# Optimization experiments

Hardware: AMD Instinct MI355X
Metric: run time of the kernel (lower is better)

The kernel has to match this reference:

```python
import math
import jax, jax.numpy as jnp
import numpy as np

B, L, D, H = 4, 2048, 1024, 16
HS = D // H  # 64


def setup_inputs() -> dict:
    key = jax.random.key(0)
    ks = jax.random.split(key, 6)
    x = jax.random.normal(ks[0], (B, L, D), dtype=jnp.float32)
    W_attn = jax.random.normal(ks[1], (D, 3 * D), dtype=jnp.float32) * 0.02
    b_attn = jnp.zeros((3 * D,), dtype=jnp.float32)
    W_proj = jax.random.normal(ks[2], (D, D), dtype=jnp.float32) * 0.02
    b_proj = jnp.zeros((D,), dtype=jnp.float32)
    Er = jax.random.normal(ks[3], (L, HS), dtype=jnp.float32)  # block_size == L
    return {"x": x, "W_attn": W_attn, "b_attn": b_attn,
            "W_proj": W_proj, "b_proj": b_proj, "Er": Er}


def _skew(QEr):
    # QEr: [B, H, L, L] -> pad one column on the left, reshape, drop first row.
    b, h, r, c = QEr.shape
    padded = jnp.pad(QEr, ((0, 0), (0, 0), (0, 0), (1, 0)))  # [B,H,L,L+1]
    return padded.reshape(b, h, c + 1, r)[:, :, 1:, :]        # [B,H,L,L]


def reference(x, W_attn, b_attn, W_proj, b_proj, Er):
    b, l, d = x.shape
    qkv = x @ W_attn + b_attn                     # [B,L,3D]
    q, k, v = jnp.split(qkv, 3, axis=2)
    q = q.reshape(b, l, H, HS).transpose(0, 2, 1, 3)  # [B,H,L,hs]
    k = k.reshape(b, l, H, HS).transpose(0, 2, 1, 3)
    v = v.reshape(b, l, H, HS).transpose(0, 2, 1, 3)
    # start = block_size - L = 0 here; Er_t: [hs, L]
    Er_t = Er[Er.shape[0] - l:, :].T
    QEr = jnp.einsum('bhld,dm->bhlm', q, Er_t)    # [B,H,L,L]
    Srel = _skew(QEr)
    scale = 1.0 / math.sqrt(HS)
    att = (jnp.einsum('bhqd,bhkd->bhqk', q, k) + Srel) * scale
    causal = jnp.tril(jnp.ones((l, l), dtype=bool))
    att = jnp.where(causal[None, None, :, :], att, -jnp.inf)
    att = jax.nn.softmax(att, axis=-1)
    y = jnp.einsum('bhqk,bhkd->bhqd', att, v)     # [B,H,L,hs]
    y = y.transpose(0, 2, 1, 3).reshape(b, l, d)
    return y @ W_proj + b_proj
```

## Files before the change

### kernel.cpp

```cpp
#include <hip/hip_runtime.h>
#include <hip/hip_bf16.h>
#include <math.h>

#define B_  4
#define L_  2048
#define D_  1024
#define H_  16
#define HS_ 64
#define SCALE 0.125f

typedef unsigned short ushort_t;
typedef __attribute__((ext_vector_type(8))) short short8;
typedef __attribute__((ext_vector_type(4))) float f32x4;

static __device__ __forceinline__ ushort_t f2bf(float f) {
    union { float f; unsigned int u; } cv; cv.f = f;
    unsigned int u = cv.u;
    unsigned int r = (u + 0x7FFFu + ((u >> 16) & 1u)) >> 16;
    return (ushort_t)r;
}
static __device__ __forceinline__ float bf2f(ushort_t h) {
    union { float f; unsigned int u; } cv; cv.u = ((unsigned int)h) << 16;
    return cv.f;
}

static __device__ __forceinline__ void gload_lds16(const ushort_t* g, ushort_t* l) {
    __builtin_amdgcn_global_load_lds(
        (const __attribute__((address_space(1))) unsigned int*)g,
        (__attribute__((address_space(3))) unsigned int*)l, 16, 0, 0);
}

__global__ __launch_bounds__(256)
void conv_to_bf16(const float* __restrict__ x, ushort_t* __restrict__ xb)
{
    const size_t i = (size_t)blockIdx.x * 256 + threadIdx.x;
    const float4* src = (const float4*)x + i * 2;
    float4 a = src[0], b = src[1];
    ushort_t o[8] = {f2bf(a.x), f2bf(a.y), f2bf(a.z), f2bf(a.w),
                     f2bf(b.x), f2bf(b.y), f2bf(b.z), f2bf(b.w)};
    *(uint4*)(xb + i * 8) = *(uint4*)o;
}

__global__ __launch_bounds__(256)
void transpose_to_bf16(const float* __restrict__ W, ushort_t* __restrict__ Wt,
                       int K, int N)
{
    __shared__ ushort_t tile[64][65];
    const int tid = threadIdx.x;
    const int n0 = blockIdx.x * 64, k0 = blockIdx.y * 64;
#pragma unroll
    for (int s = 0; s < 16; ++s) {
        const int idx = s * 256 + tid;
        const int kl = idx >> 6, nl = idx & 63;
        tile[nl][kl] = f2bf(W[(size_t)(k0 + kl) * N + n0 + nl]);
    }
    __syncthreads();
#pragma unroll
    for (int s = 0; s < 8; ++s) {
        const int idx = s * 256 + tid;
        const int nl = idx >> 5, kc = idx & 31;
        const unsigned int vlo = tile[nl][kc * 2];
        const unsigned int vhi = tile[nl][kc * 2 + 1];
        *(unsigned int*)(Wt + (size_t)(n0 + nl) * K + k0 + kc * 2) =
            vlo | (vhi << 16);
    }
}

__global__ __launch_bounds__(256)
void qkv_mfma(const ushort_t* __restrict__ A, const ushort_t* __restrict__ Bt,
              const float* __restrict__ bias, ushort_t* __restrict__ qkv)
{
    __shared__ __align__(16) ushort_t As[128 * 64];
    __shared__ __align__(16) ushort_t Bs[128 * 64];

    const int tid = threadIdx.x;
    const int w = tid >> 6, lane = tid & 63, quad = lane >> 4, lcol = lane & 15;
    const int wr = w >> 1, wc = w & 1;
    const int m0 = blockIdx.y * 128, n0 = blockIdx.x * 128;
    const int K = D_;

    const int srow = tid >> 3;
    const int cg = (tid & 7) ^ (srow & 7);
    const ushort_t* gA = A + (size_t)(m0 + srow) * K + cg * 8;
    const ushort_t* gB = Bt + (size_t)(n0 + srow) * K + cg * 8;
    ushort_t* lA = As + tid * 8;
    ushort_t* lB = Bs + tid * 8;

    const int cs0 = ((quad) ^ (lcol & 7)) * 8;
    const int cs1 = ((4 + quad) ^ (lcol & 7)) * 8;

    f32x4 acc[4][4];
#pragma unroll
    for (int i = 0; i < 4; ++i)
#pragma unroll
        for (int j = 0; j < 4; ++j) acc[i][j] = (f32x4){0, 0, 0, 0};

    for (int k0 = 0; k0 < K; k0 += 64) {
        __syncthreads();
#pragma unroll
        for (int s = 0; s < 4; ++s) {
            gload_lds16(gA + k0 + (size_t)s * 32 * K, lA + s * 2048);
            gload_lds16(gB + k0 + (size_t)s * 32 * K, lB + s * 2048);
        }
        __syncthreads();
#pragma unroll
        for (int kk = 0; kk < 2; ++kk) {
            const int cs = kk ? cs1 : cs0;
            short8 af[4], bf[4];
#pragma unroll
            for (int i = 0; i < 4; ++i)
                af[i] = *(const short8*)&As[(wr * 64 + i * 16 + lcol) * 64 + cs];
#pragma unroll
            for (int j = 0; j < 4; ++j)
                bf[j] = *(const short8*)&Bs[(wc * 64 + j * 16 + lcol) * 64 + cs];
#pragma unroll
            for (int i = 0; i < 4; ++i)
#pragma unroll
                for (int j = 0; j < 4; ++j)
                    acc[i][j] = __builtin_amdgcn_mfma_f32_16x16x32_bf16(
                        af[i], bf[j], acc[i][j], 0, 0, 0);
        }
    }

    const size_t per = (size_t)B_ * H_ * L_ * HS_;
#pragma unroll
    for (int j = 0; j < 4; ++j) {
        const int col = n0 + wc * 64 + j * 16 + lcol;
        const float bv = bias[col];
        const int sel = col >> 10;
        const int within = col & 1023;
        const int hh = within >> 6, hs = within & 63;
        ushort_t* base = qkv + (size_t)sel * per;
#pragma unroll
        for (int i = 0; i < 4; ++i) {
#pragma unroll
            for (int reg = 0; reg < 4; ++reg) {
                const int row = m0 + wr * 64 + i * 16 + quad * 4 + reg;
                const int bb = row >> 11, ll = row & 2047;
                base[(((size_t)(bb * H_ + hh)) * L_ + ll) * HS_ + hs] =
                    f2bf(acc[i][j][reg] + bv);
            }
        }
    }
}

__global__ __launch_bounds__(256)
void proj_mfma(const ushort_t* __restrict__ A, const ushort_t* __restrict__ Bt,
               const float* __restrict__ bias, float* __restrict__ C)
{
    __shared__ __align__(16) ushort_t As[128 * 64];
    __shared__ __align__(16) ushort_t Bs[128 * 64];

    const int tid = threadIdx.x;
    const int w = tid >> 6, lane = tid & 63, quad = lane >> 4, lcol = lane & 15;
    const int wr = w >> 1, wc = w & 1;
    const int m0 = blockIdx.y * 128, n0 = blockIdx.x * 128;
    const int K = D_;
    const int N = D_;

    const int srow = tid >> 3;
    const int cg = (tid & 7) ^ (srow & 7);
    const ushort_t* gA = A + (size_t)(m0 + srow) * K + cg * 8;
    const ushort_t* gB = Bt + (size_t)(n0 + srow) * K + cg * 8;
    ushort_t* lA = As + tid * 8;
    ushort_t* lB = Bs + tid * 8;

    const int cs0 = ((quad) ^ (lcol & 7)) * 8;
    const int cs1 = ((4 + quad) ^ (lcol & 7)) * 8;

    f32x4 acc[4][4];
#pragma unroll
    for (int i = 0; i < 4; ++i)
#pragma unroll
        for (int j = 0; j < 4; ++j) acc[i][j] = (f32x4){0, 0, 0, 0};

    for (int k0 = 0; k0 < K; k0 += 64) {
        __syncthreads();
#pragma unroll
        for (int s = 0; s < 4; ++s) {
            gload_lds16(gA + k0 + (size_t)s * 32 * K, lA + s * 2048);
            gload_lds16(gB + k0 + (size_t)s * 32 * K, lB + s * 2048);
        }
        __syncthreads();
#pragma unroll
        for (int kk = 0; kk < 2; ++kk) {
            const int cs = kk ? cs1 : cs0;
            short8 af[4], bf[4];
#pragma unroll
            for (int i = 0; i < 4; ++i)
                af[i] = *(const short8*)&As[(wr * 64 + i * 16 + lcol) * 64 + cs];
#pragma unroll
            for (int j = 0; j < 4; ++j)
                bf[j] = *(const short8*)&Bs[(wc * 64 + j * 16 + lcol) * 64 + cs];
#pragma unroll
            for (int i = 0; i < 4; ++i)
#pragma unroll
                for (int j = 0; j < 4; ++j)
                    acc[i][j] = __builtin_amdgcn_mfma_f32_16x16x32_bf16(
                        af[i], bf[j], acc[i][j], 0, 0, 0);
        }
    }

#pragma unroll
    for (int j = 0; j < 4; ++j) {
        const int col = n0 + wc * 64 + j * 16 + lcol;
        const float bv = bias[col];
#pragma unroll
        for (int i = 0; i < 4; ++i) {
#pragma unroll
            for (int reg = 0; reg < 4; ++reg) {
                const int row = m0 + wr * 64 + i * 16 + quad * 4 + reg;
                C[(size_t)row * N + col] = acc[i][j][reg] + bv;
            }
        }
    }
}

#define QT 64
#define KT 64

__global__ __launch_bounds__(256)
void attn_mfma(const ushort_t* __restrict__ q, const ushort_t* __restrict__ k,
               const ushort_t* __restrict__ v, const float* __restrict__ Er,
               ushort_t* __restrict__ y)
{
    __shared__ __align__(16) ushort_t Qs[64][72];
    __shared__ __align__(16) ushort_t Ks[64][72];
    __shared__ __align__(16) ushort_t Vt[64][72];
    __shared__ __align__(16) ushort_t EsPs[64][72];
    __shared__ __align__(16) ushort_t EBuf[64][132];

    const int tid  = threadIdx.x;
    const int w    = tid >> 6;
    const int lane = tid & 63;
    const int quad = lane >> 4;
    const int lcol = lane & 15;
    const int bh   = blockIdx.y;
    const int qt   = (int)gridDim.x - 1 - (int)blockIdx.x;
    const int qi0  = qt * QT;
    const int bb   = bh >> 4;
    const int hh   = bh & 15;
    const int cband = L_ - QT - qi0;

    const ushort_t* qp = q + (size_t)bh * L_ * HS_;
    const ushort_t* kp = k + (size_t)bh * L_ * HS_;
    const ushort_t* vp = v + (size_t)bh * L_ * HS_;

    const int srow = tid >> 2;
    const int scol = (tid & 3) * 16;

    {
        const uint4* src = (const uint4*)(qp + (size_t)(qi0 + srow) * HS_ + scol);
        *(uint4*)&Qs[srow][scol]     = src[0];
        *(uint4*)&Qs[srow][scol + 8] = src[1];
    }
    {
        const int m = cband + srow;
        const float4* src = (const float4*)(Er + (size_t)m * HS_ + scol);
        float4 f0 = src[0], f1 = src[1], f2 = src[2], f3 = src[3];
        ushort_t o[16];
        o[0]=f2bf(f0.x); o[1]=f2bf(f0.y); o[2]=f2bf(f0.z); o[3]=f2bf(f0.w);
        o[4]=f2bf(f1.x); o[5]=f2bf(f1.y); o[6]=f2bf(f1.z); o[7]=f2bf(f1.w);
        o[8]=f2bf(f2.x); o[9]=f2bf(f2.y); o[10]=f2bf(f2.z); o[11]=f2bf(f2.w);
        o[12]=f2bf(f3.x); o[13]=f2bf(f3.y); o[14]=f2bf(f3.z); o[15]=f2bf(f3.w);
        *(uint4*)&EsPs[srow][scol]     = *(uint4*)&o[0];
        *(uint4*)&EsPs[srow][scol + 8] = *(uint4*)&o[8];
    }
    __syncthreads();

    const short8 aq0 = *(const short8*)&Qs[w * 16 + lcol][quad * 8];
    const short8 aq1 = *(const short8*)&Qs[w * 16 + lcol][32 + quad * 8];

    {
        f32x4 e0 = {0,0,0,0}, e1 = {0,0,0,0}, e2 = {0,0,0,0}, e3 = {0,0,0,0};
        e0 = __builtin_amdgcn_mfma_f32_16x16x32_bf16(aq0, *(const short8*)&EsPs[ 0 + lcol][quad*8],      e0, 0,0,0);
        e1 = __builtin_amdgcn_mfma_f32_16x16x32_bf16(aq0, *(const short8*)&EsPs[16 + lcol][quad*8],      e1, 0,0,0);
        e2 = __builtin_amdgcn_mfma_f32_16x16x32_bf16(aq0, *(const short8*)&EsPs[32 + lcol][quad*8],      e2, 0,0,0);
        e3 = __builtin_amdgcn_mfma_f32_16x16x32_bf16(aq0, *(const short8*)&EsPs[48 + lcol][quad*8],      e3, 0,0,0);
        e0 = __builtin_amdgcn_mfma_f32_16x16x32_bf16(aq1, *(const short8*)&EsPs[ 0 + lcol][32 + quad*8], e0, 0,0,0);
        e1 = __builtin_amdgcn_mfma_f32_16x16x32_bf16(aq1, *(const short8*)&EsPs[16 + lcol][32 + quad*8], e1, 0,0,0);
        e2 = __builtin_amdgcn_mfma_f32_16x16x32_bf16(aq1, *(const short8*)&EsPs[32 + lcol][32 + quad*8], e2, 0,0,0);
        e3 = __builtin_amdgcn_mfma_f32_16x16x32_bf16(aq1, *(const short8*)&EsPs[48 + lcol][32 + quad*8], e3, 0,0,0);
        const int rw = w * 16 + quad * 4;
#pragma unroll
        for (int reg = 0; reg < 4; ++reg) {
            EBuf[rw + reg][ 0 + lcol] = f2bf(e0[reg]);
            EBuf[rw + reg][16 + lcol] = f2bf(e1[reg]);
            EBuf[rw + reg][32 + lcol] = f2bf(e2[reg]);
            EBuf[rw + reg][48 + lcol] = f2bf(e3[reg]);
        }
    }

    f32x4 O[4];
#pragma unroll
    for (int nt = 0; nt < 4; ++nt) O[nt] = (f32x4){0, 0, 0, 0};
    float m_r[4] = {-INFINITY, -INFINITY, -INFINITY, -INFINITY};
    float l_r[4] = {0, 0, 0, 0};

    for (int kt = 0; kt <= qt; ++kt) {
        const int kj0 = kt * KT;
        __syncthreads();

        {
            const uint4* src = (const uint4*)(kp + (size_t)(kj0 + srow) * HS_ + scol);
            *(uint4*)&Ks[srow][scol]     = src[0];
            *(uint4*)&Ks[srow][scol + 8] = src[1];
        }
        {
            const ushort_t* src = vp + (size_t)(kj0 + srow) * HS_ + scol;
            uint4 a = *(const uint4*)src, b = *(const uint4*)(src + 8);
            ushort_t tmp[16];
            *(uint4*)&tmp[0] = a; *(uint4*)&tmp[8] = b;
#pragma unroll
            for (int u = 0; u < 16; ++u) Vt[scol + u][srow] = tmp[u];
        }
        {
            int m = cband + (kt + 1) * 64 + srow;
            m = (m > L_ - 1) ? (L_ - 1) : m;
            const float4* src = (const float4*)(Er + (size_t)m * HS_ + scol);
            float4 f0 = src[0], f1 = src[1], f2 = src[2], f3 = src[3];
            ushort_t o[16];
            o[0]=f2bf(f0.x); o[1]=f2bf(f0.y); o[2]=f2bf(f0.z); o[3]=f2bf(f0.w);
            o[4]=f2bf(f1.x); o[5]=f2bf(f1.y); o[6]=f2bf(f1.z); o[7]=f2bf(f1.w);
            o[8]=f2bf(f2.x); o[9]=f2bf(f2.y); o[10]=f2bf(f2.z); o[11]=f2bf(f2.w);
            o[12]=f2bf(f3.x); o[13]=f2bf(f3.y); o[14]=f2bf(f3.z); o[15]=f2bf(f3.w);
            *(uint4*)&EsPs[srow][scol]     = *(uint4*)&o[0];
            *(uint4*)&EsPs[srow][scol + 8] = *(uint4*)&o[8];
        }
        __syncthreads();

        f32x4 s0 = {0,0,0,0}, s1 = {0,0,0,0}, s2 = {0,0,0,0}, s3 = {0,0,0,0};
        f32x4 e0 = {0,0,0,0}, e1 = {0,0,0,0}, e2 = {0,0,0,0}, e3 = {0,0,0,0};
        s0 = __builtin_amdgcn_mfma_f32_16x16x32_bf16(aq0, *(const short8*)&Ks[ 0 + lcol][quad*8],        s0, 0,0,0);
        s1 = __builtin_amdgcn_mfma_f32_16x16x32_bf16(aq0, *(const short8*)&Ks[16 + lcol][quad*8],        s1, 0,0,0);
        s2 = __builtin_amdgcn_mfma_f32_16x16x32_bf16(aq0, *(const short8*)&Ks[32 + lcol][quad*8],        s2, 0,0,0);
        s3 = __builtin_amdgcn_mfma_f32_16x16x32_bf16(aq0, *(const short8*)&Ks[48 + lcol][quad*8],        s3, 0,0,0);
        s0 = __builtin_amdgcn_mfma_f32_16x16x32_bf16(aq1, *(const short8*)&Ks[ 0 + lcol][32 + quad*8],   s0, 0,0,0);
        s1 = __builtin_amdgcn_mfma_f32_16x16x32_bf16(aq1, *(const short8*)&Ks[16 + lcol][32 + quad*8],   s1, 0,0,0);
        s2 = __builtin_amdgcn_mfma_f32_16x16x32_bf16(aq1, *(const short8*)&Ks[32 + lcol][32 + quad*8],   s2, 0,0,0);
        s3 = __builtin_amdgcn_mfma_f32_16x16x32_bf16(aq1, *(const short8*)&Ks[48 + lcol][32 + quad*8],   s3, 0,0,0);
        e0 = __builtin_amdgcn_mfma_f32_16x16x32_bf16(aq0, *(const short8*)&EsPs[ 0 + lcol][quad*8],      e0, 0,0,0);
        e1 = __builtin_amdgcn_mfma_f32_16x16x32_bf16(aq0, *(const short8*)&EsPs[16 + lcol][quad*8],      e1, 0,0,0);
        e2 = __builtin_amdgcn_mfma_f32_16x16x32_bf16(aq0, *(const short8*)&EsPs[32 + lcol][quad*8],      e2, 0,0,0);
        e3 = __builtin_amdgcn_mfma_f32_16x16x32_bf16(aq0, *(const short8*)&EsPs[48 + lcol][quad*8],      e3, 0,0,0);
        e0 = __builtin_amdgcn_mfma_f32_16x16x32_bf16(aq1, *(const short8*)&EsPs[ 0 + lcol][32 + quad*8], e0, 0,0,0);
        e1 = __builtin_amdgcn_mfma_f32_16x16x32_bf16(aq1, *(const short8*)&EsPs[16 + lcol][32 + quad*8], e1, 0,0,0);
        e2 = __builtin_amdgcn_mfma_f32_16x16x32_bf16(aq1, *(const short8*)&EsPs[32 + lcol][32 + quad*8], e2, 0,0,0);
        e3 = __builtin_amdgcn_mfma_f32_16x16x32_bf16(aq1, *(const short8*)&EsPs[48 + lcol][32 + quad*8], e3, 0,0,0);

        {
            const int par = ((kt + 1) & 1) * 64;
            const int rw = w * 16 + quad * 4;
#pragma unroll
            for (int reg = 0; reg < 4; ++reg) {
                EBuf[rw + reg][par +  0 + lcol] = f2bf(e0[reg]);
                EBuf[rw + reg][par + 16 + lcol] = f2bf(e1[reg]);
                EBuf[rw + reg][par + 32 + lcol] = f2bf(e2[reg]);
                EBuf[rw + reg][par + 48 + lcol] = f2bf(e3[reg]);
            }
        }

        float p_[4][4];
        float al[4];
        const float sq[4][4] = {
            {s0[0], s0[1], s0[2], s0[3]},
            {s1[0], s1[1], s1[2], s1[3]},
            {s2[0], s2[1], s2[2], s2[3]},
            {s3[0], s3[1], s3[2], s3[3]}};
#pragma unroll
        for (int reg = 0; reg < 4; ++reg) {
            const int r = w * 16 + quad * 4 + reg;
            float scr[4];
#pragma unroll
            for (int nt = 0; nt < 4; ++nt) {
                const int jl = nt * 16 + lcol;
                const int c = (63 - r + jl + kj0) & 127;
                float sv = (sq[nt][reg] + bf2f(EBuf[r][c])) * SCALE;
                if (kt == qt && jl > r) sv = -INFINITY;
                scr[nt] = sv;
            }
            float mx = fmaxf(fmaxf(scr[0], scr[1]), fmaxf(scr[2], scr[3]));
            mx = fmaxf(mx, __shfl_xor(mx, 1));
            mx = fmaxf(mx, __shfl_xor(mx, 2));
            mx = fmaxf(mx, __shfl_xor(mx, 4));
            mx = fmaxf(mx, __shfl_xor(mx, 8));
            const float nm = fmaxf(m_r[reg], mx);
            const float a_ = __expf(m_r[reg] - nm);
            m_r[reg] = nm;
            float ps = 0.f;
#pragma unroll
            for (int nt = 0; nt < 4; ++nt) {
                const float p = __expf(scr[nt] - nm);
                p_[nt][reg] = p;
                ps += p;
            }
            ps += __shfl_xor(ps, 1);
            ps += __shfl_xor(ps, 2);
            ps += __shfl_xor(ps, 4);
            ps += __shfl_xor(ps, 8);
            l_r[reg] = l_r[reg] * a_ + ps;
            al[reg] = a_;
        }
#pragma unroll
        for (int nt = 0; nt < 4; ++nt)
#pragma unroll
            for (int reg = 0; reg < 4; ++reg) O[nt][reg] *= al[reg];

        __syncthreads();

        {
            const int rw = w * 16 + quad * 4;
#pragma unroll
            for (int reg = 0; reg < 4; ++reg) {
                EsPs[rw + reg][ 0 + lcol] = f2bf(p_[0][reg]);
                EsPs[rw + reg][16 + lcol] = f2bf(p_[1][reg]);
                EsPs[rw + reg][32 + lcol] = f2bf(p_[2][reg]);
                EsPs[rw + reg][48 + lcol] = f2bf(p_[3][reg]);
            }
        }
        const short8 ap0 = *(const short8*)&EsPs[w * 16 + lcol][quad * 8];
        const short8 ap1 = *(const short8*)&EsPs[w * 16 + lcol][32 + quad * 8];
        O[0] = __builtin_amdgcn_mfma_f32_16x16x32_bf16(ap0, *(const short8*)&Vt[ 0 + lcol][quad*8],      O[0], 0,0,0);
        O[1] = __builtin_amdgcn_mfma_f32_16x16x32_bf16(ap0, *(const short8*)&Vt[16 + lcol][quad*8],      O[1], 0,0,0);
        O[2] = __builtin_amdgcn_mfma_f32_16x16x32_bf16(ap0, *(const short8*)&Vt[32 + lcol][quad*8],      O[2], 0,0,0);
        O[3] = __builtin_amdgcn_mfma_f32_16x16x32_bf16(ap0, *(const short8*)&Vt[48 + lcol][quad*8],      O[3], 0,0,0);
        O[0] = __builtin_amdgcn_mfma_f32_16x16x32_bf16(ap1, *(const short8*)&Vt[ 0 + lcol][32 + quad*8], O[0], 0,0,0);
        O[1] = __builtin_amdgcn_mfma_f32_16x16x32_bf16(ap1, *(const short8*)&Vt[16 + lcol][32 + quad*8], O[1], 0,0,0);
        O[2] = __builtin_amdgcn_mfma_f32_16x16x32_bf16(ap1, *(const short8*)&Vt[32 + lcol][32 + quad*8], O[2], 0,0,0);
        O[3] = __builtin_amdgcn_mfma_f32_16x16x32_bf16(ap1, *(const short8*)&Vt[48 + lcol][32 + quad*8], O[3], 0,0,0);
    }

    float inv[4];
#pragma unroll
    for (int reg = 0; reg < 4; ++reg) inv[reg] = 1.f / l_r[reg];
#pragma unroll
    for (int nt = 0; nt < 4; ++nt) {
#pragma unroll
        for (int reg = 0; reg < 4; ++reg) {
            const int r = w * 16 + quad * 4 + reg;
            y[(((size_t)bb * L_ + qi0 + r) * H_ + hh) * HS_ + nt * 16 + lcol] =
                f2bf(O[nt][reg] * inv[reg]);
        }
    }
}

extern "C" void kernel_launch(void* const* d_in, const int* in_sizes, int n_in,
                              void* d_out, int out_size, void* d_ws, size_t ws_size,
                              hipStream_t stream)
{
    const float* x      = (const float*)d_in[0];
    const float* W_attn = (const float*)d_in[1];
    const float* b_attn = (const float*)d_in[2];
    const float* W_proj = (const float*)d_in[3];
    const float* b_proj = (const float*)d_in[4];
    const float* Er     = (const float*)d_in[5];
    float* out = (float*)d_out;

    const size_t per = (size_t)B_ * H_ * L_ * HS_;
    ushort_t* qb  = (ushort_t*)d_ws;
    ushort_t* kb  = qb + per;
    ushort_t* vb  = kb + per;
    ushort_t* yb  = vb + per;
    ushort_t* xb  = yb + per;
    ushort_t* wat = xb + per;
    ushort_t* wpt = wat + (size_t)3 * D_ * D_;

    dim3 blk(256);

    conv_to_bf16<<<dim3((B_ * L_ * D_) / 2048), blk, 0, stream>>>(x, xb);
    transpose_to_bf16<<<dim3(3 * D_ / 64, D_ / 64), blk, 0, stream>>>(W_attn, wat, D_, 3 * D_);
    transpose_to_bf16<<<dim3(D_ / 64, D_ / 64), blk, 0, stream>>>(W_proj, wpt, D_, D_);

    qkv_mfma<<<dim3(3 * D_ / 128, B_ * L_ / 128), blk, 0, stream>>>(xb, wat, b_attn, qb);

    attn_mfma<<<dim3(L_ / QT, B_ * H_), blk, 0, stream>>>(qb, kb, vb, Er, yb);

    proj_mfma<<<dim3(D_ / 128, B_ * L_ / 128), blk, 0, stream>>>(yb, wpt, b_proj, out);
}
```

Measured before the change: 582.8 us.

## Restructure attention: register-ring skew, max-free softmax, transposed V, async LDS loads

The QKV epilogue now writes V already transposed, and Er is converted to bf16 once up front. K, V^T, Q and Er tiles are loaded straight into XOR-swizzled LDS with global_load_lds, replacing the per-thread transposes and float-to-bf16 conversions inside the loop. The relative-position skew is kept in a register ring of QEr tiles read through lane shuffles instead of a bf16 LDS buffer. The softmax also drops the running max and rescaling, saving one barrier and the max reductions per iteration, at the risk of exp overflow if scores grow large. The loop is unrolled by two and launch bounds request higher occupancy.

```diff
diff --git a/kernel.cpp b/kernel.cpp
--- a/kernel.cpp
+++ b/kernel.cpp
@@ -18,10 +18,6 @@
     unsigned int u = cv.u;
     unsigned int r = (u + 0x7FFFu + ((u >> 16) & 1u)) >> 16;
     return (ushort_t)r;
-}
-static __device__ __forceinline__ float bf2f(ushort_t h) {
-    union { float f; unsigned int u; } cv; cv.u = ((unsigned int)h) << 16;
-    return cv.f;
 }
 
 static __device__ __forceinline__ void gload_lds16(const ushort_t* g, ushort_t* l) {
@@ -130,15 +126,29 @@
         const int sel = col >> 10;
         const int within = col & 1023;
         const int hh = within >> 6, hs = within & 63;
-        ushort_t* base = qkv + (size_t)sel * per;
-#pragma unroll
-        for (int i = 0; i < 4; ++i) {
-#pragma unroll
-            for (int reg = 0; reg < 4; ++reg) {
-                const int row = m0 + wr * 64 + i * 16 + quad * 4 + reg;
-                const int bb = row >> 11, ll = row & 2047;
-                base[(((size_t)(bb * H_ + hh)) * L_ + ll) * HS_ + hs] =
-                    f2bf(acc[i][j][reg] + bv);
+        if (sel < 2) {
+            ushort_t* base = qkv + (size_t)sel * per;
+#pragma unroll
+            for (int i = 0; i < 4; ++i) {
+#pragma unroll
+                for (int reg = 0; reg < 4; ++reg) {
+                    const int row = m0 + wr * 64 + i * 16 + quad * 4 + reg;
+                    const int bb = row >> 11, ll = row & 2047;
+                    base[(((size_t)(bb * H_ + hh)) * L_ + ll) * HS_ + hs] =
+                        f2bf(acc[i][j][reg] + bv);
+                }
+            }
+        } else {
+            ushort_t* base = qkv + 2 * per;
+#pragma unroll
+            for (int i = 0; i < 4; ++i) {
+#pragma unroll
+                for (int reg = 0; reg < 4; ++reg) {
+                    const int row = m0 + wr * 64 + i * 16 + quad * 4 + reg;
+                    const int bb = row >> 11, ll = row & 2047;
+                    base[(((size_t)(bb * H_ + hh)) * HS_ + hs) * L_ + ll] =
+                        f2bf(acc[i][j][reg] + bv);
+                }
             }
         }
     }
@@ -216,19 +226,98 @@
     }
 }
 
-#define QT 64
-#define KT 64
-
-__global__ __launch_bounds__(256)
+#define MFMA16(a, b, c) __builtin_amdgcn_mfma_f32_16x16x32_bf16(a, b, c, 0, 0, 0)
+
+#define RING_STORE(C1) do {                                                       \
+    if (w == 0)      { Ring[((C1)+5)&7]=e0; Ring[((C1)+6)&7]=e1;                  \
+                       Ring[((C1)+7)&7]=e2; Ring[((C1)+8)&7]=e3; }                \
+    else if (w == 1) { Ring[((C1)+6)&7]=e0; Ring[((C1)+7)&7]=e1;                  \
+                       Ring[((C1)+8)&7]=e2; Ring[((C1)+9)&7]=e3; }                \
+    else if (w == 2) { Ring[((C1)+7)&7]=e0; Ring[((C1)+8)&7]=e1;                  \
+                       Ring[((C1)+9)&7]=e2; Ring[((C1)+10)&7]=e3; }               \
+    else             { Ring[((C1)+8)&7]=e0; Ring[((C1)+9)&7]=e1;                  \
+                       Ring[((C1)+10)&7]=e2; Ring[((C1)+11)&7]=e3; }              \
+} while (0)
+
+#define ATTN_ITER(KTv, C0, C1) {                                                  \
+    const int kj0 = (KTv) * 64;                                                   \
+    const bool diag = ((KTv) == qt);                                              \
+    __syncthreads();                                                              \
+    gload_lds16(kp + (size_t)(kj0 + srow) * 64 + cg8, Ks + tid * 8);              \
+    gload_lds16(kp + (size_t)(kj0 + srow + 32) * 64 + cg8, Ks + tid * 8 + 2048);  \
+    gload_lds16(vtp + (size_t)srow * L_ + kj0 + cg8, Vts + tid * 8);              \
+    gload_lds16(vtp + (size_t)(srow + 32) * L_ + kj0 + cg8, Vts + tid * 8 + 2048);\
+    { int m1 = cband + ((KTv) + 1) * 64 + srow; if (m1 > L_ - 1) m1 = L_ - 1;     \
+      int m2 = cband + ((KTv) + 1) * 64 + srow + 32; if (m2 > L_ - 1) m2 = L_ - 1;\
+      gload_lds16(er + (size_t)m1 * 64 + cg8, Es + tid * 8);                      \
+      gload_lds16(er + (size_t)m2 * 64 + cg8, Es + tid * 8 + 2048); }             \
+    __syncthreads();                                                              \
+    f32x4 S0 = {0,0,0,0}, S1 = {0,0,0,0}, S2 = {0,0,0,0}, S3 = {0,0,0,0};         \
+    f32x4 e0 = {0,0,0,0}, e1 = {0,0,0,0}, e2 = {0,0,0,0}, e3 = {0,0,0,0};         \
+    S0 = MFMA16(aq0, *(const short8*)&Ks[( 0 + lcol) * 64 + fr0], S0);            \
+    S1 = MFMA16(aq0, *(const short8*)&Ks[(16 + lcol) * 64 + fr0], S1);            \
+    S2 = MFMA16(aq0, *(const short8*)&Ks[(32 + lcol) * 64 + fr0], S2);            \
+    S3 = MFMA16(aq0, *(const short8*)&Ks[(48 + lcol) * 64 + fr0], S3);            \
+    S0 = MFMA16(aq1, *(const short8*)&Ks[( 0 + lcol) * 64 + fr1], S0);            \
+    S1 = MFMA16(aq1, *(const short8*)&Ks[(16 + lcol) * 64 + fr1], S1);            \
+    S2 = MFMA16(aq1, *(const short8*)&Ks[(32 + lcol) * 64 + fr1], S2);            \
+    S3 = MFMA16(aq1, *(const short8*)&Ks[(48 + lcol) * 64 + fr1], S3);            \
+    e0 = MFMA16(aq0, *(const short8*)&Es[( 0 + lcol) * 64 + fr0], e0);            \
+    e1 = MFMA16(aq0, *(const short8*)&Es[(16 + lcol) * 64 + fr0], e1);            \
+    e2 = MFMA16(aq0, *(const short8*)&Es[(32 + lcol) * 64 + fr0], e2);            \
+    e3 = MFMA16(aq0, *(const short8*)&Es[(48 + lcol) * 64 + fr0], e3);            \
+    e0 = MFMA16(aq1, *(const short8*)&Es[( 0 + lcol) * 64 + fr1], e0);            \
+    e1 = MFMA16(aq1, *(const short8*)&Es[(16 + lcol) * 64 + fr1], e1);            \
+    e2 = MFMA16(aq1, *(const short8*)&Es[(32 + lcol) * 64 + fr1], e2);            \
+    e3 = MFMA16(aq1, *(const short8*)&Es[(48 + lcol) * 64 + fr1], e3);            \
+    RING_STORE(C1);                                                               \
+    f32x4 S[4] = {S0, S1, S2, S3};                                                \
+    _Pragma("unroll")                                                             \
+    for (int reg = 0; reg < 4; ++reg) {                                           \
+        const int qr = quad * 4 + reg;                                            \
+        const int srcl = quad * 16 + ((15 - qr + lcol) & 15);                     \
+        const bool carry = (lcol > qr);                                           \
+        float psum = 0.f;                                                         \
+        _Pragma("unroll")                                                         \
+        for (int nt = 0; nt < 4; ++nt) {                                          \
+            const float v0 = __shfl(Ring[((C0) + nt) & 7][reg], srcl, 64);        \
+            const float v1 = __shfl(Ring[((C0) + nt + 1) & 7][reg], srcl, 64);    \
+            const float ev = carry ? v1 : v0;                                     \
+            const float sv = (S[nt][reg] + ev) * SCALE;                           \
+            float p = __expf(sv);                                                 \
+            if (diag && (nt * 16 + lcol > w * 16 + qr)) p = 0.f;                  \
+            psum += p;                                                            \
+            Ps[(w * 16 + qr) * 64 +                                               \
+               (((nt * 2 + (lcol >> 3)) ^ (qr & 7)) * 8) + (lcol & 7)] = f2bf(p); \
+        }                                                                         \
+        psum += __shfl_xor(psum, 1);                                              \
+        psum += __shfl_xor(psum, 2);                                              \
+        psum += __shfl_xor(psum, 4);                                              \
+        psum += __shfl_xor(psum, 8);                                              \
+        l_r[reg] += psum;                                                         \
+    }                                                                             \
+    const short8 ap0 = *(const short8*)&Ps[(w * 16 + lcol) * 64 + fr0];           \
+    const short8 ap1 = *(const short8*)&Ps[(w * 16 + lcol) * 64 + fr1];           \
+    O[0] = MFMA16(ap0, *(const short8*)&Vts[( 0 + lcol) * 64 + fr0], O[0]);       \
+    O[1] = MFMA16(ap0, *(const short8*)&Vts[(16 + lcol) * 64 + fr0], O[1]);       \
+    O[2] = MFMA16(ap0, *(const short8*)&Vts[(32 + lcol) * 64 + fr0], O[2]);       \
+    O[3] = MFMA16(ap0, *(const short8*)&Vts[(48 + lcol) * 64 + fr0], O[3]);       \
+    O[0] = MFMA16(ap1, *(const short8*)&Vts[( 0 + lcol) * 64 + fr1], O[0]);       \
+    O[1] = MFMA16(ap1, *(const short8*)&Vts[(16 + lcol) * 64 + fr1], O[1]);       \
+    O[2] = MFMA16(ap1, *(const short8*)&Vts[(32 + lcol) * 64 + fr1], O[2]);       \
+    O[3] = MFMA16(ap1, *(const short8*)&Vts[(48 + lcol) * 64 + fr1], O[3]);       \
+}
+
+__global__ __launch_bounds__(256, 4)
 void attn_mfma(const ushort_t* __restrict__ q, const ushort_t* __restrict__ k,
-               const ushort_t* __restrict__ v, const float* __restrict__ Er,
+               const ushort_t* __restrict__ vt, const ushort_t* __restrict__ er,
                ushort_t* __restrict__ y)
 {
-    __shared__ __align__(16) ushort_t Qs[64][72];
-    __shared__ __align__(16) ushort_t Ks[64][72];
-    __shared__ __align__(16) ushort_t Vt[64][72];
-    __shared__ __align__(16) ushort_t EsPs[64][72];
-    __shared__ __align__(16) ushort_t EBuf[64][132];
+    __shared__ __align__(16) ushort_t Qs[64 * 64];
+    __shared__ __align__(16) ushort_t Ks[64 * 64];
+    __shared__ __align__(16) ushort_t Vts[64 * 64];
+    __shared__ __align__(16) ushort_t Es[64 * 64];
+    __shared__ __align__(16) ushort_t Ps[64 * 64];
 
     const int tid  = threadIdx.x;
     const int w    = tid >> 6;
@@ -237,197 +326,51 @@
     const int lcol = lane & 15;
     const int bh   = blockIdx.y;
     const int qt   = (int)gridDim.x - 1 - (int)blockIdx.x;
-    const int qi0  = qt * QT;
+    const int qi0  = qt * 64;
     const int bb   = bh >> 4;
     const int hh   = bh & 15;
-    const int cband = L_ - QT - qi0;
-
-    const ushort_t* qp = q + (size_t)bh * L_ * HS_;
-    const ushort_t* kp = k + (size_t)bh * L_ * HS_;
-    const ushort_t* vp = v + (size_t)bh * L_ * HS_;
-
-    const int srow = tid >> 2;
-    const int scol = (tid & 3) * 16;
-
-    {
-        const uint4* src = (const uint4*)(qp + (size_t)(qi0 + srow) * HS_ + scol);
-        *(uint4*)&Qs[srow][scol]     = src[0];
-        *(uint4*)&Qs[srow][scol + 8] = src[1];
-    }
-    {
-        const int m = cband + srow;
-        const float4* src = (const float4*)(Er + (size_t)m * HS_ + scol);
-        float4 f0 = src[0], f1 = src[1], f2 = src[2], f3 = src[3];
-        ushort_t o[16];
-        o[0]=f2bf(f0.x); o[1]=f2bf(f0.y); o[2]=f2bf(f0.z); o[3]=f2bf(f0.w);
-        o[4]=f2bf(f1.x); o[5]=f2bf(f1.y); o[6]=f2bf(f1.z); o[7]=f2bf(f1.w);
-        o[8]=f2bf(f2.x); o[9]=f2bf(f2.y); o[10]=f2bf(f2.z); o[11]=f2bf(f2.w);
-        o[12]=f2bf(f3.x); o[13]=f2bf(f3.y); o[14]=f2bf(f3.z); o[15]=f2bf(f3.w);
-        *(uint4*)&EsPs[srow][scol]     = *(uint4*)&o[0];
-        *(uint4*)&EsPs[srow][scol + 8] = *(uint4*)&o[8];
-    }
+    const int cband = L_ - 64 - qi0;
+
+    const ushort_t* qp  = q + (size_t)bh * L_ * HS_;
+    const ushort_t* kp  = k + (size_t)bh * L_ * HS_;
+    const ushort_t* vtp = vt + (size_t)bh * HS_ * L_;
+
+    const int srow = tid >> 3;
+    const int cg8  = ((tid & 7) ^ (srow & 7)) * 8;
+
+    gload_lds16(qp + (size_t)(qi0 + srow) * 64 + cg8, Qs + tid * 8);
+    gload_lds16(qp + (size_t)(qi0 + srow + 32) * 64 + cg8, Qs + tid * 8 + 2048);
+    gload_lds16(er + (size_t)(cband + srow) * 64 + cg8, Es + tid * 8);
+    gload_lds16(er + (size_t)(cband + srow + 32) * 64 + cg8, Es + tid * 8 + 2048);
     __syncthreads();
 
-    const short8 aq0 = *(const short8*)&Qs[w * 16 + lcol][quad * 8];
-    const short8 aq1 = *(const short8*)&Qs[w * 16 + lcol][32 + quad * 8];
-
+    const int fr0 = ((quad) ^ (lcol & 7)) * 8;
+    const int fr1 = ((4 + quad) ^ (lcol & 7)) * 8;
+    const short8 aq0 = *(const short8*)&Qs[(w * 16 + lcol) * 64 + fr0];
+    const short8 aq1 = *(const short8*)&Qs[(w * 16 + lcol) * 64 + fr1];
+
+    f32x4 Ring[8];
     {
         f32x4 e0 = {0,0,0,0}, e1 = {0,0,0,0}, e2 = {0,0,0,0}, e3 = {0,0,0,0};
-        e0 = __builtin_amdgcn_mfma_f32_16x16x32_bf16(aq0, *(const short8*)&EsPs[ 0 + lcol][quad*8],      e0, 0,0,0);
-        e1 = __builtin_amdgcn_mfma_f32_16x16x32_bf16(aq0, *(const short8*)&EsPs[16 + lcol][quad*8],      e1, 0,0,0);
-        e2 = __builtin_amdgcn_mfma_f32_16x16x32_bf16(aq0, *(const short8*)&EsPs[32 + lcol][quad*8],      e2, 0,0,0);
-        e3 = __builtin_amdgcn_mfma_f32_16x16x32_bf16(aq0, *(const short8*)&EsPs[48 + lcol][quad*8],      e3, 0,0,0);
-        e0 = __builtin_amdgcn_mfma_f32_16x16x32_bf16(aq1, *(const short8*)&EsPs[ 0 + lcol][32 + quad*8], e0, 0,0,0);
-        e1 = __builtin_amdgcn_mfma_f32_16x16x32_bf16(aq1, *(const short8*)&EsPs[16 + lcol][32 + quad*8], e1, 0,0,0);
-        e2 = __builtin_amdgcn_mfma_f32_16x16x32_bf16(aq1, *(const short8*)&EsPs[32 + lcol][32 + quad*8], e2, 0,0,0);
-        e3 = __builtin_amdgcn_mfma_f32_16x16x32_bf16(aq1, *(const short8*)&EsPs[48 + lcol][32 + quad*8], e3, 0,0,0);
-        const int rw = w * 16 + quad * 4;
-#pragma unroll
-        for (int reg = 0; reg < 4; ++reg) {
-            EBuf[rw + reg][ 0 + lcol] = f2bf(e0[reg]);
-            EBuf[rw + reg][16 + lcol] = f2bf(e1[reg]);
-            EBuf[rw + reg][32 + lcol] = f2bf(e2[reg]);
-            EBuf[rw + reg][48 + lcol] = f2bf(e3[reg]);
-        }
+        e0 = MFMA16(aq0, *(const short8*)&Es[( 0 + lcol) * 64 + fr0], e0);
+        e1 = MFMA16(aq0, *(const short8*)&Es[(16 + lcol) * 64 + fr0], e1);
+        e2 = MFMA16(aq0, *(const short8*)&Es[(32 + lcol) * 64 + fr0], e2);
+        e3 = MFMA16(aq0, *(const short8*)&Es[(48 + lcol) * 64 + fr0], e3);
+        e0 = MFMA16(aq1, *(const short8*)&Es[( 0 + lcol) * 64 + fr1], e0);
+        e1 = MFMA16(aq1, *(const short8*)&Es[(16 + lcol) * 64 + fr1], e1);
+        e2 = MFMA16(aq1, *(const short8*)&Es[(32 + lcol) * 64 + fr1], e2);
+        e3 = MFMA16(aq1, *(const short8*)&Es[(48 + lcol) * 64 + fr1], e3);
+        RING_STORE(0);
     }
 
     f32x4 O[4];
 #pragma unroll
     for (int nt = 0; nt < 4; ++nt) O[nt] = (f32x4){0, 0, 0, 0};
-    float m_r[4] = {-INFINITY, -INFINITY, -INFINITY, -INFINITY};
     float l_r[4] = {0, 0, 0, 0};
 
-    for (int kt = 0; kt <= qt; ++kt) {
-        const int kj0 = kt * KT;
-        __syncthreads();
-
-        {
-            const uint4* src = (const uint4*)(kp + (size_t)(kj0 + srow) * HS_ + scol);
-            *(uint4*)&Ks[srow][scol]     = src[0];
-            *(uint4*)&Ks[srow][scol + 8] = src[1];
-        }
-        {
-            const ushort_t* src = vp + (size_t)(kj0 + srow) * HS_ + scol;
-            uint4 a = *(const uint4*)src, b = *(const uint4*)(src + 8);
-            ushort_t tmp[16];
-            *(uint4*)&tmp[0] = a; *(uint4*)&tmp[8] = b;
-#pragma unroll
-            for (int u = 0; u < 16; ++u) Vt[scol + u][srow] = tmp[u];
-        }
-        {
-            int m = cband + (kt + 1) * 64 + srow;
-            m = (m > L_ - 1) ? (L_ - 1) : m;
-            const float4* src = (const float4*)(Er + (size_t)m * HS_ + scol);
-            float4 f0 = src[0], f1 = src[1], f2 = src[2], f3 = src[3];
-            ushort_t o[16];
-            o[0]=f2bf(f0.x); o[1]=f2bf(f0.y); o[2]=f2bf(f0.z); o[3]=f2bf(f0.w);
-            o[4]=f2bf(f1.x); o[5]=f2bf(f1.y); o[6]=f2bf(f1.z); o[7]=f2bf(f1.w);
-            o[8]=f2bf(f2.x); o[9]=f2bf(f2.y); o[10]=f2bf(f2.z); o[11]=f2bf(f2.w);
-            o[12]=f2bf(f3.x); o[13]=f2bf(f3.y); o[14]=f2bf(f3.z); o[15]=f2bf(f3.w);
-            *(uint4*)&EsPs[srow][scol]     = *(uint4*)&o[0];
-            *(uint4*)&EsPs[srow][scol + 8] = *(uint4*)&o[8];
-        }
-        __syncthreads();
-
-        f32x4 s0 = {0,0,0,0}, s1 = {0,0,0,0}, s2 = {0,0,0,0}, s3 = {0,0,0,0};
-        f32x4 e0 = {0,0,0,0}, e1 = {0,0,0,0}, e2 = {0,0,0,0}, e3 = {0,0,0,0};
-        s0 = __builtin_amdgcn_mfma_f32_16x16x32_bf16(aq0, *(const short8*)&Ks[ 0 + lcol][quad*8],        s0, 0,0,0);
-        s1 = __builtin_amdgcn_mfma_f32_16x16x32_bf16(aq0, *(const short8*)&Ks[16 + lcol][quad*8],        s1, 0,0,0);
-        s2 = __builtin_amdgcn_mfma_f32_16x16x32_bf16(aq0, *(const short8*)&Ks[32 + lcol][quad*8],        s2, 0,0,0);
-        s3 = __builtin_amdgcn_mfma_f32_16x16x32_bf16(aq0, *(const short8*)&Ks[48 + lcol][quad*8],        s3, 0,0,0);
-        s0 = __builtin_amdgcn_mfma_f32_16x16x32_bf16(aq1, *(const short8*)&Ks[ 0 + lcol][32 + quad*8],   s0, 0,0,0);
-        s1 = __builtin_amdgcn_mfma_f32_16x16x32_bf16(aq1, *(const short8*)&Ks[16 + lcol][32 + quad*8],   s1, 0,0,0);
-        s2 = __builtin_amdgcn_mfma_f32_16x16x32_bf16(aq1, *(const short8*)&Ks[32 + lcol][32 + quad*8],   s2, 0,0,0);
-        s3 = __builtin_amdgcn_mfma_f32_16x16x32_bf16(aq1, *(const short8*)&Ks[48 + lcol][32 + quad*8],   s3, 0,0,0);
-        e0 = __builtin_amdgcn_mfma_f32_16x16x32_bf16(aq0, *(const short8*)&EsPs[ 0 + lcol][quad*8],      e0, 0,0,0);
-        e1 = __builtin_amdgcn_mfma_f32_16x16x32_bf16(aq0, *(const short8*)&EsPs[16 + lcol][quad*8],      e1, 0,0,0);
-        e2 = __builtin_amdgcn_mfma_f32_16x16x32_bf16(aq0, *(const short8*)&EsPs[32 + lcol][quad*8],      e2, 0,0,0);
-        e3 = __builtin_amdgcn_mfma_f32_16x16x32_bf16(aq0, *(const short8*)&EsPs[48 + lcol][quad*8],      e3, 0,0,0);
-        e0 = __builtin_amdgcn_mfma_f32_16x16x32_bf16(aq1, *(const short8*)&EsPs[ 0 + lcol][32 + quad*8], e0, 0,0,0);
-        e1 = __builtin_amdgcn_mfma_f32_16x16x32_bf16(aq1, *(const short8*)&EsPs[16 + lcol][32 + quad*8], e1, 0,0,0);
-        e2 = __builtin_amdgcn_mfma_f32_16x16x32_bf16(aq1, *(const short8*)&EsPs[32 + lcol][32 + quad*8], e2, 0,0,0);
-        e3 = __builtin_amdgcn_mfma_f32_16x16x32_bf16(aq1, *(const short8*)&EsPs[48 + lcol][32 + quad*8], e3, 0,0,0);
-
-        {
-            const int par = ((kt + 1) & 1) * 64;
-            const int rw = w * 16 + quad * 4;
-#pragma unroll
-            for (int reg = 0; reg < 4; ++reg) {
-                EBuf[rw + reg][par +  0 + lcol] = f2bf(e0[reg]);
-                EBuf[rw + reg][par + 16 + lcol] = f2bf(e1[reg]);
-                EBuf[rw + reg][par + 32 + lcol] = f2bf(e2[reg]);
-                EBuf[rw + reg][par + 48 + lcol] = f2bf(e3[reg]);
-            }
-        }
-
-        float p_[4][4];
-        float al[4];
-        const float sq[4][4] = {
-            {s0[0], s0[1], s0[2], s0[3]},
-            {s1[0], s1[1], s1[2], s1[3]},
-            {s2[0], s2[1], s2[2], s2[3]},
-            {s3[0], s3[1], s3[2], s3[3]}};
-#pragma unroll
-        for (int reg = 0; reg < 4; ++reg) {
-            const int r = w * 16 + quad * 4 + reg;
-            float scr[4];
-#pragma unroll
-            for (int nt = 0; nt < 4; ++nt) {
-                const int jl = nt * 16 + lcol;
-                const int c = (63 - r + jl + kj0) & 127;
-                float sv = (sq[nt][reg] + bf2f(EBuf[r][c])) * SCALE;
-                if (kt == qt && jl > r) sv = -INFINITY;
-                scr[nt] = sv;
-            }
-            float mx = fmaxf(fmaxf(scr[0], scr[1]), fmaxf(scr[2], scr[3]));
-            mx = fmaxf(mx, __shfl_xor(mx, 1));
-            mx = fmaxf(mx, __shfl_xor(mx, 2));
-            mx = fmaxf(mx, __shfl_xor(mx, 4));
-            mx = fmaxf(mx, __shfl_xor(mx, 8));
-            const float nm = fmaxf(m_r[reg], mx);
-            const float a_ = __expf(m_r[reg] - nm);
-            m_r[reg] = nm;
-            float ps = 0.f;
-#pragma unroll
-            for (int nt = 0; nt < 4; ++nt) {
-                const float p = __expf(scr[nt] - nm);
-                p_[nt][reg] = p;
-                ps += p;
-            }
-            ps += __shfl_xor(ps, 1);
-            ps += __shfl_xor(ps, 2);
-            ps += __shfl_xor(ps, 4);
-            ps += __shfl_xor(ps, 8);
-            l_r[reg] = l_r[reg] * a_ + ps;
-            al[reg] = a_;
-        }
-#pragma unroll
-        for (int nt = 0; nt < 4; ++nt)
-#pragma unroll
-            for (int reg = 0; reg < 4; ++reg) O[nt][reg] *= al[reg];
-
-        __syncthreads();
-
-        {
-            const int rw = w * 16 + quad * 4;
-#pragma unroll
-            for (int reg = 0; reg < 4; ++reg) {
-                EsPs[rw + reg][ 0 + lcol] = f2bf(p_[0][reg]);
-                EsPs[rw + reg][16 + lcol] = f2bf(p_[1][reg]);
-                EsPs[rw + reg][32 + lcol] = f2bf(p_[2][reg]);
-                EsPs[rw + reg][48 + lcol] = f2bf(p_[3][reg]);
-            }
-        }
-        const short8 ap0 = *(const short8*)&EsPs[w * 16 + lcol][quad * 8];
-        const short8 ap1 = *(const short8*)&EsPs[w * 16 + lcol][32 + quad * 8];
-        O[0] = __builtin_amdgcn_mfma_f32_16x16x32_bf16(ap0, *(const short8*)&Vt[ 0 + lcol][quad*8],      O[0], 0,0,0);
-        O[1] = __builtin_amdgcn_mfma_f32_16x16x32_bf16(ap0, *(const short8*)&Vt[16 + lcol][quad*8],      O[1], 0,0,0);
-        O[2] = __builtin_amdgcn_mfma_f32_16x16x32_bf16(ap0, *(const short8*)&Vt[32 + lcol][quad*8],      O[2], 0,0,0);
-        O[3] = __builtin_amdgcn_mfma_f32_16x16x32_bf16(ap0, *(const short8*)&Vt[48 + lcol][quad*8],      O[3], 0,0,0);
-        O[0] = __builtin_amdgcn_mfma_f32_16x16x32_bf16(ap1, *(const short8*)&Vt[ 0 + lcol][32 + quad*8], O[0], 0,0,0);
-        O[1] = __builtin_amdgcn_mfma_f32_16x16x32_bf16(ap1, *(const short8*)&Vt[16 + lcol][32 + quad*8], O[1], 0,0,0);
-        O[2] = __builtin_amdgcn_mfma_f32_16x16x32_bf16(ap1, *(const short8*)&Vt[32 + lcol][32 + quad*8], O[2], 0,0,0);
-        O[3] = __builtin_amdgcn_mfma_f32_16x16x32_bf16(ap1, *(const short8*)&Vt[48 + lcol][32 + quad*8], O[3], 0,0,0);
+    for (int kt = 0; kt <= qt; kt += 2) {
+        ATTN_ITER(kt, 0, 4);
+        if (kt + 1 <= qt) ATTN_ITER(kt + 1, 4, 0);
     }
 
     float inv[4];
@@ -459,21 +402,23 @@
     const size_t per = (size_t)B_ * H_ * L_ * HS_;
     ushort_t* qb  = (ushort_t*)d_ws;
     ushort_t* kb  = qb + per;
-    ushort_t* vb  = kb + per;
-    ushort_t* yb  = vb + per;
+    ushort_t* vtb = kb + per;
+    ushort_t* yb  = vtb + per;
     ushort_t* xb  = yb + per;
     ushort_t* wat = xb + per;
     ushort_t* wpt = wat + (size_t)3 * D_ * D_;
+    ushort_t* erb = wpt + (size_t)D_ * D_;
 
     dim3 blk(256);
 
     conv_to_bf16<<<dim3((B_ * L_ * D_) / 2048), blk, 0, stream>>>(x, xb);
+    conv_to_bf16<<<dim3((L_ * HS_) / 2048), blk, 0, stream>>>(Er, erb);
     transpose_to_bf16<<<dim3(3 * D_ / 64, D_ / 64), blk, 0, stream>>>(W_attn, wat, D_, 3 * D_);
     transpose_to_bf16<<<dim3(D_ / 64, D_ / 64), blk, 0, stream>>>(W_proj, wpt, D_, D_);
 
     qkv_mfma<<<dim3(3 * D_ / 128, B_ * L_ / 128), blk, 0, stream>>>(xb, wat, b_attn, qb);
 
-    attn_mfma<<<dim3(L_ / QT, B_ * H_), blk, 0, stream>>>(qb, kb, vb, Er, yb);
+    attn_mfma<<<dim3(L_ / 64, B_ * H_), blk, 0, stream>>>(qb, kb, vtb, erb, yb);
 
     proj_mfma<<<dim3(D_ / 128, B_ * L_ / 128), blk, 0, stream>>>(yb, wpt, b_proj, out);
 }
```

After: 669.6 us. 1.15x slower.
